# Kernel optimization log

Measured on AMD Instinct MI355X. Metric: run time of the kernel, lower is better.

The kernel has to match this reference:

```python
import jax, jax.numpy as jnp
import numpy as np

B, S, D, H, V, DFF, L, MAXLEN = 256, 64, 1024, 16, 64, 4096, 8, 64
HD = D // H
SCALE = HD ** -0.5
EPS = 1e-5


def _ln(x, g, b):
    m = jnp.mean(x, axis=-1, keepdims=True)
    v = jnp.mean((x - m) ** 2, axis=-1, keepdims=True)
    return (x - m) * jax.lax.rsqrt(v + EPS) * g + b


def setup_inputs() -> dict:
    key = jax.random.key(0)
    ks = jax.random.split(key, 12)
    n = lambda k, shape: jax.random.normal(k, shape, jnp.float32) * 0.02
    return {
        "x": jax.random.randint(ks[0], (B, S), 0, V + 1),
        "step": 0,
        "token_embed": n(ks[1], (V + 1, D)),
        "step_embed": n(ks[2], (MAXLEN, D)),
        "qkv_w": n(ks[3], (L, 3 * D, D)),
        "qkv_b": jnp.zeros((L, 3 * D), jnp.float32),
        "out_w": n(ks[4], (L, D, D)),
        "out_b": jnp.zeros((L, D), jnp.float32),
        "rel_bias": n(ks[5], (L, 2 * MAXLEN - 1)),
        "w1": n(ks[6], (L, DFF, D)),
        "b1": jnp.zeros((L, DFF), jnp.float32),
        "w2": n(ks[7], (L, D, DFF)),
        "b2": jnp.zeros((L, D), jnp.float32),
        "ln1_g": jnp.ones((L, D), jnp.float32),
        "ln1_b": jnp.zeros((L, D), jnp.float32),
        "ln2_g": jnp.ones((L, D), jnp.float32),
        "ln2_b": jnp.zeros((L, D), jnp.float32),
        "lno_g": jnp.ones((D,), jnp.float32),
        "lno_b": jnp.zeros((D,), jnp.float32),
        "pol_w": n(ks[8], (V, D)),
        "pol_b": jnp.zeros((V,), jnp.float32),
        "val_w": n(ks[9], (1, D)),
        "val_b": jnp.zeros((1,), jnp.float32),
    }


def _forward(x, step, token_embed, step_embed, qkv_w, qkv_b, out_w, out_b,
             rel_bias, w1, b1, w2, b2, ln1_g, ln1_b, ln2_g, ln2_b,
             lno_g, lno_b, pol_w, pol_b, val_w, val_b):
    h = token_embed[x]  # [B,S,D]
    step_idx = min(int(step), MAXLEN - 1)
    h = h + step_embed[step_idx][None, None, :]

    pos = jnp.arange(S)
    rel_idx = jnp.clip(pos[:, None] - pos[None, :] + (MAXLEN - 1), 0, 2 * MAXLEN - 2)  # [S,S]

    def layer(h, p):
        qw, qb, ow, ob, rb, w1_, b1_, w2_, b2_, g1, be1, g2, be2 = p
        qkv = h @ qw.T + qb  # [B,S,3D]
        qkv = qkv.reshape(B, S, 3, H, HD).transpose(2, 0, 3, 1, 4)
        q, k, v = qkv[0], qkv[1], qkv[2]  # [B,H,S,HD]
        scores = jnp.einsum('bhqd,bhkd->bhqk', q, k) * SCALE + rb[rel_idx][None, None]
        probs = jax.nn.softmax(scores, axis=-1)
        attn = jnp.einsum('bhqk,bhkd->bhqd', probs, v)  # [B,H,S,HD]
        attn = attn.transpose(0, 2, 1, 3).reshape(B, S, D) @ ow.T + ob
        h = _ln(h + attn, g1, be1)
        ffn = jax.nn.gelu(h @ w1_.T + b1_, approximate=False) @ w2_.T + b2_
        h = _ln(h + ffn, g2, be2)
        return h, None

    h, _ = jax.lax.scan(layer, h, (qkv_w, qkv_b, out_w, out_b, rel_bias,
                                   w1, b1, w2, b2, ln1_g, ln1_b, ln2_g, ln2_b))
    h = _ln(h, lno_g, lno_b)
    pooled = h.mean(axis=1)  # [B,D]
    policy = pooled @ pol_w.T + pol_b  # [B,V]
    value = pooled @ val_w.T + val_b   # [B,1]
    return policy, value, h


def reference(x, step, token_embed, step_embed, qkv_w, qkv_b, out_w, out_b,
              rel_bias, w1, b1, w2, b2, ln1_g, ln1_b, ln2_g, ln2_b,
              lno_g, lno_b, pol_w, pol_b, val_w, val_b):
    return _forward(x, step, token_embed, step_embed, qkv_w, qkv_b, out_w, out_b,
                    rel_bias, w1, b1, w2, b2, ln1_g, ln1_b, ln2_g, ln2_b,
                    lno_g, lno_b, pol_w, pol_b, val_w, val_b)
```

## Files before the change

kernel.cpp:

```cpp
#include <hip/hip_runtime.h>
#include <math.h>

typedef _Float16 f16;
typedef _Float16 f16x8 __attribute__((ext_vector_type(8)));
typedef _Float16 f16x4 __attribute__((ext_vector_type(4)));
typedef float floatx4 __attribute__((ext_vector_type(4)));

#define BATCH 256
#define SEQ 64
#define DMODEL 1024
#define NHEAD 16
#define HDIM 64
#define VOCAB 64
#define DFF 4096
#define NLAYER 8
#define MS (BATCH*SEQ)

#define GPTR(p) ((const __attribute__((address_space(1))) void*)(p))
#define LPTR(p) ((__attribute__((address_space(3))) void*)(p))

__device__ __forceinline__ floatx4 mfma16(f16x8 a, f16x8 b, floatx4 c) {
    return __builtin_amdgcn_mfma_f32_16x16x32_f16(a, b, c, 0, 0, 0);
}

__device__ __forceinline__ float gelu_f(float x) {
    return 0.5f * x * (1.f + erff(x * 0.70710678118654752f));
}

__global__ __launch_bounds__(256) void embed_k(const int* __restrict__ x, const int* __restrict__ step,
                                               const float* __restrict__ tok, const float* __restrict__ se,
                                               float* __restrict__ h, f16* __restrict__ hb) {
    int row = blockIdx.x;
    int t = threadIdx.x;
    int id = x[row];
    int si = min(max(step[0], 0), 63);
    float4 a = ((const float4*)(tok + (size_t)id * DMODEL))[t];
    float4 b = ((const float4*)(se + (size_t)si * DMODEL))[t];
    float4 o;
    o.x = a.x + b.x; o.y = a.y + b.y; o.z = a.z + b.z; o.w = a.w + b.w;
    ((float4*)(h + (size_t)row * DMODEL))[t] = o;
    f16x4 hv; hv[0] = (f16)o.x; hv[1] = (f16)o.y; hv[2] = (f16)o.z; hv[3] = (f16)o.w;
    ((f16x4*)(hb + (size_t)row * DMODEL))[t] = hv;
}

__global__ __launch_bounds__(256) void cvt_k(const float* __restrict__ src, f16* __restrict__ dst, int n4) {
    int i = blockIdx.x * 256 + threadIdx.x;
    if (i < n4) {
        float4 v = ((const float4*)src)[i];
        f16x4 o; o[0] = (f16)v.x; o[1] = (f16)v.y; o[2] = (f16)v.z; o[3] = (f16)v.w;
        ((f16x4*)dst)[i] = o;
    }
}

template<int MODE>
__global__ __launch_bounds__(256, 2) void gemm_k(const f16* __restrict__ A, const f16* __restrict__ Bw,
                                                 const float* __restrict__ bias,
                                                 f16* __restrict__ Cb, float* __restrict__ Hacc,
                                                 int M, int N, int K) {
    __shared__ f16 smem[32768];

    const int tid = threadIdx.x;
    const int lane = tid & 63;
    const int wave = tid >> 6;
    const int wm = wave >> 1, wn = wave & 1;
    const int lr = lane & 15, lg = lane >> 4;
    const int sa = lr & 7;

    const unsigned nx = gridDim.x;
    const unsigned nwg = nx * gridDim.y;
    unsigned flat = blockIdx.y * nx + blockIdx.x;
    flat = (flat & 7u) * (nwg >> 3) + (flat >> 3);
    const int m0 = (int)(flat / nx) * 128;
    const int n0 = (int)(flat % nx) * 128;

    floatx4 acc[4][4] = {};

    const int srow = tid >> 3;
    const int scbs = (tid & 7) ^ (srow & 7);
    const f16* Asrc = A + (size_t)(m0 + srow) * K + scbs * 8;
    const f16* Bsrc = Bw + (size_t)(n0 + srow) * K + scbs * 8;
    const int ldsw = wave * 512;

#define STAGE(bi, tt) do {                                                                        \
    const f16* _a = Asrc + (size_t)(tt) * 64;                                                     \
    const f16* _b = Bsrc + (size_t)(tt) * 64;                                                     \
    f16* _l = smem + ((bi) << 14) + ldsw;                                                         \
    __builtin_amdgcn_global_load_lds(GPTR(_a),                  LPTR(_l),         16, 0, 0);      \
    __builtin_amdgcn_global_load_lds(GPTR(_a + 32 * (size_t)K), LPTR(_l + 2048),  16, 0, 0);      \
    __builtin_amdgcn_global_load_lds(GPTR(_a + 64 * (size_t)K), LPTR(_l + 4096),  16, 0, 0);      \
    __builtin_amdgcn_global_load_lds(GPTR(_a + 96 * (size_t)K), LPTR(_l + 6144),  16, 0, 0);      \
    __builtin_amdgcn_global_load_lds(GPTR(_b),                  LPTR(_l + 8192),  16, 0, 0);      \
    __builtin_amdgcn_global_load_lds(GPTR(_b + 32 * (size_t)K), LPTR(_l + 10240), 16, 0, 0);      \
    __builtin_amdgcn_global_load_lds(GPTR(_b + 64 * (size_t)K), LPTR(_l + 12288), 16, 0, 0);      \
    __builtin_amdgcn_global_load_lds(GPTR(_b + 96 * (size_t)K), LPTR(_l + 14336), 16, 0, 0);      \
} while (0)

    const int NT = K >> 6;

    STAGE(0, 0);
    asm volatile("s_waitcnt vmcnt(0)" ::: "memory");
    __builtin_amdgcn_s_barrier();

    int buf = 0;
    for (int t = 0; t < NT; ++t) {
        if (t + 1 < NT) STAGE(buf ^ 1, t + 1);

        const f16* Ab = smem + (buf << 14);
        const f16* Bb = Ab + 8192;
        f16x8 af[8], bf[8];
#pragma unroll
        for (int kh = 0; kh < 2; ++kh)
#pragma unroll
            for (int mi = 0; mi < 4; ++mi)
                af[kh * 4 + mi] = *(const f16x8*)(Ab + (wm * 64 + mi * 16 + lr) * 64
                                                  + (((kh * 4 + lg) ^ sa) << 3));
#pragma unroll
        for (int kh = 0; kh < 2; ++kh)
#pragma unroll
            for (int ni = 0; ni < 4; ++ni)
                bf[kh * 4 + ni] = *(const f16x8*)(Bb + (wn * 64 + ni * 16 + lr) * 64
                                                  + (((kh * 4 + lg) ^ sa) << 3));

        __builtin_amdgcn_s_setprio(1);
#pragma unroll
        for (int kh = 0; kh < 2; ++kh)
#pragma unroll
            for (int mi = 0; mi < 4; ++mi)
#pragma unroll
                for (int ni = 0; ni < 4; ++ni)
                    acc[mi][ni] = mfma16(af[kh * 4 + mi], bf[kh * 4 + ni], acc[mi][ni]);
        __builtin_amdgcn_s_setprio(0);

        if (t + 1 < NT) { asm volatile("s_waitcnt vmcnt(0)" ::: "memory"); }
        __builtin_amdgcn_s_barrier();
        buf ^= 1;
    }
#undef STAGE

    if (MODE == 2) {
#pragma unroll
        for (int ni = 0; ni < 4; ++ni) {
            int cc = n0 + wn * 64 + ni * 16 + lr;
            float bvl = bias[cc];
#pragma unroll
            for (int mi = 0; mi < 4; ++mi)
#pragma unroll
                for (int j = 0; j < 4; ++j) {
                    int rr = m0 + wm * 64 + mi * 16 + lg * 4 + j;
                    float* p = Hacc + (size_t)rr * N + cc;
                    *p += acc[mi][ni][j] + bvl;
                }
        }
    } else {
        f16* scr = smem + wave * 4096;
        float bsv[4];
#pragma unroll
        for (int ni = 0; ni < 4; ++ni) bsv[ni] = bias[n0 + wn * 64 + ni * 16 + lr];
#pragma unroll
        for (int mi = 0; mi < 4; ++mi)
#pragma unroll
            for (int ni = 0; ni < 4; ++ni)
#pragma unroll
                for (int j = 0; j < 4; ++j) {
                    int r = mi * 16 + lg * 4 + j;
                    int c = ni * 16 + lr;
                    float v = acc[mi][ni][j] + bsv[ni];
                    if (MODE == 1) v = gelu_f(v);
                    scr[r * 64 + (((c >> 3) ^ (r & 7)) * 8) + (c & 7)] = (f16)v;
                }
        int gr = m0 + wm * 64 + lane;
        f16* dst = Cb + (size_t)gr * N + n0 + wn * 64;
#pragma unroll
        for (int i = 0; i < 8; ++i) {
            f16x8 v = *(const f16x8*)(scr + lane * 64 + ((i ^ (lane & 7)) * 8));
            *(f16x8*)(dst + i * 8) = v;
        }
    }
}

__global__ __launch_bounds__(64) void attn_k(const f16* __restrict__ qkv, const float* __restrict__ rb,
                                             f16* __restrict__ ctx) {
    const int hh = blockIdx.x;
    const int bb = blockIdx.y;
    const int lane = threadIdx.x;
    __shared__ float rbs[128];
    __shared__ f16 Vt[64][72];
    __shared__ f16 Pl[64][72];

    for (int i = lane; i < 127; i += 64) rbs[i] = rb[i];

    const f16* vrow = qkv + (size_t)(bb * 64 + lane) * 3072 + 2048 + hh * 64;
#pragma unroll
    for (int i = 0; i < 8; ++i) {
        f16x8 v = *(const f16x8*)(vrow + i * 8);
#pragma unroll
        for (int j = 0; j < 8; ++j) Vt[i * 8 + j][lane] = v[j];
    }
    __syncthreads();

    const int lr = lane & 15, lg = lane >> 4;
    floatx4 sacc[4][4] = {};
    const f16* qbase = qkv + (size_t)(bb * 64) * 3072 + hh * 64;
#pragma unroll
    for (int kk = 0; kk < 64; kk += 32) {
        f16x8 qa[4], kb[4];
#pragma unroll
        for (int mf = 0; mf < 4; ++mf)
            qa[mf] = *(const f16x8*)(qbase + (size_t)(mf * 16 + lr) * 3072 + kk + lg * 8);
#pragma unroll
        for (int nf = 0; nf < 4; ++nf)
            kb[nf] = *(const f16x8*)(qbase + 1024 + (size_t)(nf * 16 + lr) * 3072 + kk + lg * 8);
#pragma unroll
        for (int mf = 0; mf < 4; ++mf)
#pragma unroll
            for (int nf = 0; nf < 4; ++nf)
                sacc[mf][nf] = mfma16(qa[mf], kb[nf], sacc[mf][nf]);
    }

#pragma unroll
    for (int mf = 0; mf < 4; ++mf) {
#pragma unroll
        for (int j = 0; j < 4; ++j) {
            int qrow = mf * 16 + lg * 4 + j;
            float v0 = sacc[mf][0][j] * 0.125f + rbs[qrow - (0  + lr) + 63];
            float v1 = sacc[mf][1][j] * 0.125f + rbs[qrow - (16 + lr) + 63];
            float v2 = sacc[mf][2][j] * 0.125f + rbs[qrow - (32 + lr) + 63];
            float v3 = sacc[mf][3][j] * 0.125f + rbs[qrow - (48 + lr) + 63];
            float mx = fmaxf(fmaxf(v0, v1), fmaxf(v2, v3));
            for (int m = 1; m < 16; m <<= 1) mx = fmaxf(mx, __shfl_xor(mx, m));
            v0 = __expf(v0 - mx); v1 = __expf(v1 - mx); v2 = __expf(v2 - mx); v3 = __expf(v3 - mx);
            float sum = v0 + v1 + v2 + v3;
            for (int m = 1; m < 16; m <<= 1) sum += __shfl_xor(sum, m);
            float inv = 1.f / sum;
            Pl[qrow][0  + lr] = (f16)(v0 * inv);
            Pl[qrow][16 + lr] = (f16)(v1 * inv);
            Pl[qrow][32 + lr] = (f16)(v2 * inv);
            Pl[qrow][48 + lr] = (f16)(v3 * inv);
        }
    }
    __syncthreads();

    floatx4 oacc[4][4] = {};
#pragma unroll
    for (int kk = 0; kk < 64; kk += 32) {
        f16x8 pa[4], vb[4];
#pragma unroll
        for (int mf = 0; mf < 4; ++mf) pa[mf] = *(const f16x8*)&Pl[mf * 16 + lr][kk + lg * 8];
#pragma unroll
        for (int nf = 0; nf < 4; ++nf) vb[nf] = *(const f16x8*)&Vt[nf * 16 + lr][kk + lg * 8];
#pragma unroll
        for (int mf = 0; mf < 4; ++mf)
#pragma unroll
            for (int nf = 0; nf < 4; ++nf)
                oacc[mf][nf] = mfma16(pa[mf], vb[nf], oacc[mf][nf]);
    }
    __syncthreads();
#pragma unroll
    for (int mf = 0; mf < 4; ++mf)
#pragma unroll
        for (int nf = 0; nf < 4; ++nf)
#pragma unroll
            for (int j = 0; j < 4; ++j)
                Pl[mf * 16 + lg * 4 + j][nf * 16 + lr] = (f16)oacc[mf][nf][j];
    __syncthreads();
    f16* crow = ctx + (size_t)(bb * 64 + lane) * DMODEL + hh * 64;
#pragma unroll
    for (int i = 0; i < 8; ++i) {
        f16x8 v = *(const f16x8*)&Pl[lane][i * 8];
        *(f16x8*)(crow + i * 8) = v;
    }
}

__global__ __launch_bounds__(256) void ln_k(float* __restrict__ h, const float* __restrict__ g,
                                            const float* __restrict__ b, f16* __restrict__ hb, int emit) {
    int row = blockIdx.x;
    int t = threadIdx.x;
    float4 v = ((const float4*)(h + (size_t)row * DMODEL))[t];
    float s = v.x + v.y + v.z + v.w;
    float ss = v.x * v.x + v.y * v.y + v.z * v.z + v.w * v.w;
    for (int m = 1; m < 64; m <<= 1) { s += __shfl_xor(s, m); ss += __shfl_xor(ss, m); }
    __shared__ float red[8];
    if ((t & 63) == 0) { red[(t >> 6) * 2] = s; red[(t >> 6) * 2 + 1] = ss; }
    __syncthreads();
    s = red[0] + red[2] + red[4] + red[6];
    ss = red[1] + red[3] + red[5] + red[7];
    float mean = s * (1.f / 1024.f);
    float var = ss * (1.f / 1024.f) - mean * mean;
    float rstd = rsqrtf(var + 1e-5f);
    float4 gg = ((const float4*)g)[t];
    float4 bb = ((const float4*)b)[t];
    float4 o;
    o.x = (v.x - mean) * rstd * gg.x + bb.x;
    o.y = (v.y - mean) * rstd * gg.y + bb.y;
    o.z = (v.z - mean) * rstd * gg.z + bb.z;
    o.w = (v.w - mean) * rstd * gg.w + bb.w;
    ((float4*)(h + (size_t)row * DMODEL))[t] = o;
    if (emit) {
        f16x4 hv; hv[0] = (f16)o.x; hv[1] = (f16)o.y; hv[2] = (f16)o.z; hv[3] = (f16)o.w;
        ((f16x4*)(hb + (size_t)row * DMODEL))[t] = hv;
    }
}

__global__ __launch_bounds__(256) void pool_k(const float* __restrict__ h, float* __restrict__ pooled) {
    int b = blockIdx.x;
    int t = threadIdx.x;
    float sx = 0, sy = 0, sz = 0, sw = 0;
    for (int s = 0; s < SEQ; ++s) {
        float4 v = ((const float4*)(h + (size_t)(b * SEQ + s) * DMODEL))[t];
        sx += v.x; sy += v.y; sz += v.z; sw += v.w;
    }
    float4 o; o.x = sx * (1.f / 64.f); o.y = sy * (1.f / 64.f); o.z = sz * (1.f / 64.f); o.w = sw * (1.f / 64.f);
    ((float4*)(pooled + (size_t)b * DMODEL))[t] = o;
}

__global__ __launch_bounds__(64) void head_k(const float* __restrict__ pooled, const float* __restrict__ pw,
                                             const float* __restrict__ pb, const float* __restrict__ vw,
                                             const float* __restrict__ vb, float* __restrict__ out) {
    int b = blockIdx.x;
    int lane = threadIdx.x;
    const float* pr = pooled + (size_t)b * DMODEL;
    const float* wr = pw + (size_t)lane * DMODEL;
    float accp = 0.f;
    for (int d = 0; d < DMODEL; d += 4) {
        float4 x = *(const float4*)(pr + d);
        float4 w = *(const float4*)(wr + d);
        accp += x.x * w.x + x.y * w.y + x.z * w.z + x.w * w.w;
    }
    float accv = 0.f;
    for (int d = lane * 4; d < DMODEL; d += 256) {
        float4 x = *(const float4*)(pr + d);
        float4 w = *(const float4*)(vw + d);
        accv += x.x * w.x + x.y * w.y + x.z * w.z + x.w * w.w;
    }
    for (int m = 1; m < 64; m <<= 1) accv += __shfl_xor(accv, m);
    out[b * VOCAB + lane] = accp + pb[lane];
    if (lane == 0) out[BATCH * VOCAB + b] = accv + vb[0];
}

extern "C" void kernel_launch(void* const* d_in, const int* in_sizes, int n_in,
                              void* d_out, int out_size, void* d_ws, size_t ws_size,
                              hipStream_t stream) {
    const int*   x      = (const int*)d_in[0];
    const int*   step   = (const int*)d_in[1];
    const float* tok    = (const float*)d_in[2];
    const float* se     = (const float*)d_in[3];
    const float* qkv_w  = (const float*)d_in[4];
    const float* qkv_b  = (const float*)d_in[5];
    const float* out_w  = (const float*)d_in[6];
    const float* out_b  = (const float*)d_in[7];
    const float* relb   = (const float*)d_in[8];
    const float* w1     = (const float*)d_in[9];
    const float* b1     = (const float*)d_in[10];
    const float* w2     = (const float*)d_in[11];
    const float* b2     = (const float*)d_in[12];
    const float* ln1g   = (const float*)d_in[13];
    const float* ln1b   = (const float*)d_in[14];
    const float* ln2g   = (const float*)d_in[15];
    const float* ln2b   = (const float*)d_in[16];
    const float* lnog   = (const float*)d_in[17];
    const float* lnob   = (const float*)d_in[18];
    const float* pw     = (const float*)d_in[19];
    const float* pb     = (const float*)d_in[20];
    const float* vw     = (const float*)d_in[21];
    const float* vb     = (const float*)d_in[22];

    float* out = (float*)d_out;
    float* h = out + BATCH * VOCAB + BATCH;

    char* ws = (char*)d_ws;
    f16* hb     = (f16*)(ws);
    f16* uni    = (f16*)(ws + 33554432);
    f16* qkv16  = uni;
    f16* ffn16  = uni;
    f16* ctx16  = (f16*)(ws + 167772160);
    f16* wqb    = (f16*)(ws + 201326592);
    f16* wob    = (f16*)(ws + 207618048);
    f16* w1b    = (f16*)(ws + 209715200);
    f16* w2b    = (f16*)(ws + 218103808);
    float* pooled = (float*)(ws + 226492416);

    embed_k<<<MS, 256, 0, stream>>>(x, step, tok, se, h, hb);

    for (int l = 0; l < NLAYER; ++l) {
        cvt_k<<<3072, 256, 0, stream>>>(qkv_w + (size_t)l * 3145728, wqb, 786432);
        cvt_k<<<1024, 256, 0, stream>>>(out_w + (size_t)l * 1048576, wob, 262144);
        cvt_k<<<4096, 256, 0, stream>>>(w1 + (size_t)l * 4194304, w1b, 1048576);
        cvt_k<<<4096, 256, 0, stream>>>(w2 + (size_t)l * 4194304, w2b, 1048576);

        gemm_k<0><<<dim3(24, 128), 256, 0, stream>>>(hb, wqb, qkv_b + l * 3072, qkv16, nullptr, MS, 3072, 1024);
        attn_k<<<dim3(NHEAD, BATCH), 64, 0, stream>>>(qkv16, relb + l * 127, ctx16);
        gemm_k<2><<<dim3(8, 128), 256, 0, stream>>>(ctx16, wob, out_b + l * 1024, nullptr, h, MS, 1024, 1024);
        ln_k<<<MS, 256, 0, stream>>>(h, ln1g + l * 1024, ln1b + l * 1024, hb, 1);
        gemm_k<1><<<dim3(32, 128), 256, 0, stream>>>(hb, w1b, b1 + l * 4096, ffn16, nullptr, MS, 4096, 1024);
        gemm_k<2><<<dim3(8, 128), 256, 0, stream>>>(ffn16, w2b, b2 + l * 1024, nullptr, h, MS, 1024, 4096);
        ln_k<<<MS, 256, 0, stream>>>(h, ln2g + l * 1024, ln2b + l * 1024, hb, 1);
    }

    ln_k<<<MS, 256, 0, stream>>>(h, lnog, lnob, hb, 0);
    pool_k<<<BATCH, 256, 0, stream>>>(h, pooled);
    head_k<<<BATCH, 64, 0, stream>>>(pooled, pw, pb, vw, vb, out);
}
```

Baseline: 5.818 ms.

## Keep residual stream in fp16 and fuse layernorm statistics into GEMM epilogue

```diff
diff --git a/kernel.cpp b/kernel.cpp
--- a/kernel.cpp
+++ b/kernel.cpp
@@ -29,33 +29,39 @@
 
 __global__ __launch_bounds__(256) void embed_k(const int* __restrict__ x, const int* __restrict__ step,
                                                const float* __restrict__ tok, const float* __restrict__ se,
-                                               float* __restrict__ h, f16* __restrict__ hb) {
+                                               f16* __restrict__ r) {
     int row = blockIdx.x;
     int t = threadIdx.x;
     int id = x[row];
     int si = min(max(step[0], 0), 63);
     float4 a = ((const float4*)(tok + (size_t)id * DMODEL))[t];
     float4 b = ((const float4*)(se + (size_t)si * DMODEL))[t];
-    float4 o;
-    o.x = a.x + b.x; o.y = a.y + b.y; o.z = a.z + b.z; o.w = a.w + b.w;
-    ((float4*)(h + (size_t)row * DMODEL))[t] = o;
-    f16x4 hv; hv[0] = (f16)o.x; hv[1] = (f16)o.y; hv[2] = (f16)o.z; hv[3] = (f16)o.w;
-    ((f16x4*)(hb + (size_t)row * DMODEL))[t] = hv;
-}
-
-__global__ __launch_bounds__(256) void cvt_k(const float* __restrict__ src, f16* __restrict__ dst, int n4) {
-    int i = blockIdx.x * 256 + threadIdx.x;
-    if (i < n4) {
-        float4 v = ((const float4*)src)[i];
-        f16x4 o; o[0] = (f16)v.x; o[1] = (f16)v.y; o[2] = (f16)v.z; o[3] = (f16)v.w;
-        ((f16x4*)dst)[i] = o;
-    }
+    f16x4 hv; hv[0] = (f16)(a.x + b.x); hv[1] = (f16)(a.y + b.y);
+    hv[2] = (f16)(a.z + b.z); hv[3] = (f16)(a.w + b.w);
+    ((f16x4*)(r + (size_t)row * DMODEL))[t] = hv;
+}
+
+__global__ __launch_bounds__(256) void cvt4_k(const float* __restrict__ qw, const float* __restrict__ ow,
+                                              const float* __restrict__ w1, const float* __restrict__ w2,
+                                              f16* __restrict__ dq, f16* __restrict__ dO,
+                                              f16* __restrict__ d1, f16* __restrict__ d2) {
+    int gid = blockIdx.x * 256 + threadIdx.x;
+    const float4* s; f16x4* d; int off;
+    if (gid < 786432)        { s = (const float4*)qw; d = (f16x4*)dq; off = gid; }
+    else if (gid < 1048576)  { s = (const float4*)ow; d = (f16x4*)dO; off = gid - 786432; }
+    else if (gid < 2097152)  { s = (const float4*)w1; d = (f16x4*)d1; off = gid - 1048576; }
+    else                     { s = (const float4*)w2; d = (f16x4*)d2; off = gid - 2097152; }
+    float4 v = s[off];
+    f16x4 o; o[0] = (f16)v.x; o[1] = (f16)v.y; o[2] = (f16)v.z; o[3] = (f16)v.w;
+    d[off] = o;
 }
 
 template<int MODE>
 __global__ __launch_bounds__(256, 2) void gemm_k(const f16* __restrict__ A, const f16* __restrict__ Bw,
                                                  const float* __restrict__ bias,
-                                                 f16* __restrict__ Cb, float* __restrict__ Hacc,
+                                                 f16* __restrict__ Cb,
+                                                 const f16* __restrict__ Rres, f16* __restrict__ ResOut,
+                                                 float2* __restrict__ Part,
                                                  int M, int N, int K) {
     __shared__ f16 smem[32768];
 
@@ -95,61 +101,81 @@
     __builtin_amdgcn_global_load_lds(GPTR(_b + 96 * (size_t)K), LPTR(_l + 14336), 16, 0, 0);      \
 } while (0)
 
+#define TILE_BODY(t_, bi) do {                                                                    \
+    if ((t_) + 1 < NT) STAGE((bi) ^ 1, (t_) + 1);                                                 \
+    const f16* Ab = smem + ((bi) << 14);                                                          \
+    const f16* Bb = Ab + 8192;                                                                    \
+    f16x8 af[8], bf[8];                                                                           \
+    _Pragma("unroll") for (int kh = 0; kh < 2; ++kh)                                              \
+    _Pragma("unroll") for (int mi = 0; mi < 4; ++mi)                                              \
+        af[kh * 4 + mi] = *(const f16x8*)(Ab + (wm * 64 + mi * 16 + lr) * 64                      \
+                                          + (((kh * 4 + lg) ^ sa) << 3));                         \
+    _Pragma("unroll") for (int kh = 0; kh < 2; ++kh)                                              \
+    _Pragma("unroll") for (int ni = 0; ni < 4; ++ni)                                              \
+        bf[kh * 4 + ni] = *(const f16x8*)(Bb + (wn * 64 + ni * 16 + lr) * 64                      \
+                                          + (((kh * 4 + lg) ^ sa) << 3));                         \
+    __builtin_amdgcn_s_setprio(1);                                                                \
+    _Pragma("unroll") for (int kh = 0; kh < 2; ++kh)                                              \
+    _Pragma("unroll") for (int mi = 0; mi < 4; ++mi)                                              \
+    _Pragma("unroll") for (int ni = 0; ni < 4; ++ni)                                              \
+        acc[mi][ni] = mfma16(af[kh * 4 + mi], bf[kh * 4 + ni], acc[mi][ni]);                      \
+    __builtin_amdgcn_s_setprio(0);                                                                \
+    if ((t_) + 1 < NT) { asm volatile("s_waitcnt vmcnt(0)" ::: "memory"); }                       \
+    __builtin_amdgcn_s_barrier();                                                                 \
+} while (0)
+
     const int NT = K >> 6;
 
     STAGE(0, 0);
     asm volatile("s_waitcnt vmcnt(0)" ::: "memory");
     __builtin_amdgcn_s_barrier();
 
-    int buf = 0;
-    for (int t = 0; t < NT; ++t) {
-        if (t + 1 < NT) STAGE(buf ^ 1, t + 1);
-
-        const f16* Ab = smem + (buf << 14);
-        const f16* Bb = Ab + 8192;
-        f16x8 af[8], bf[8];
-#pragma unroll
-        for (int kh = 0; kh < 2; ++kh)
-#pragma unroll
-            for (int mi = 0; mi < 4; ++mi)
-                af[kh * 4 + mi] = *(const f16x8*)(Ab + (wm * 64 + mi * 16 + lr) * 64
-                                                  + (((kh * 4 + lg) ^ sa) << 3));
-#pragma unroll
-        for (int kh = 0; kh < 2; ++kh)
+    for (int t = 0; t < NT; t += 2) {
+        TILE_BODY(t, 0);
+        TILE_BODY(t + 1, 1);
+    }
+#undef STAGE
+#undef TILE_BODY
+
+    if (MODE == 2) {
+        float bsv[4];
+#pragma unroll
+        for (int ni = 0; ni < 4; ++ni) bsv[ni] = bias[n0 + wn * 64 + ni * 16 + lr];
+        f16* scr = smem + wave * 4096;
+#pragma unroll
+        for (int mi = 0; mi < 4; ++mi)
 #pragma unroll
             for (int ni = 0; ni < 4; ++ni)
-                bf[kh * 4 + ni] = *(const f16x8*)(Bb + (wn * 64 + ni * 16 + lr) * 64
-                                                  + (((kh * 4 + lg) ^ sa) << 3));
-
-        __builtin_amdgcn_s_setprio(1);
-#pragma unroll
-        for (int kh = 0; kh < 2; ++kh)
-#pragma unroll
-            for (int mi = 0; mi < 4; ++mi)
-#pragma unroll
-                for (int ni = 0; ni < 4; ++ni)
-                    acc[mi][ni] = mfma16(af[kh * 4 + mi], bf[kh * 4 + ni], acc[mi][ni]);
-        __builtin_amdgcn_s_setprio(0);
-
-        if (t + 1 < NT) { asm volatile("s_waitcnt vmcnt(0)" ::: "memory"); }
-        __builtin_amdgcn_s_barrier();
-        buf ^= 1;
-    }
-#undef STAGE
-
-    if (MODE == 2) {
-#pragma unroll
-        for (int ni = 0; ni < 4; ++ni) {
-            int cc = n0 + wn * 64 + ni * 16 + lr;
-            float bvl = bias[cc];
-#pragma unroll
-            for (int mi = 0; mi < 4; ++mi)
 #pragma unroll
                 for (int j = 0; j < 4; ++j) {
-                    int rr = m0 + wm * 64 + mi * 16 + lg * 4 + j;
-                    float* p = Hacc + (size_t)rr * N + cc;
-                    *p += acc[mi][ni][j] + bvl;
+                    int rr = mi * 16 + lg * 4 + j;
+                    int cc = ni * 16 + lr;
+                    scr[rr * 64 + (((cc >> 3) ^ (rr & 7)) * 8) + (cc & 7)]
+                        = (f16)(acc[mi][ni][j] + bsv[ni]);
                 }
+        int gr = m0 + wm * 64 + lane;
+        const f16* rrow = Rres + (size_t)gr * N + n0 + wn * 64;
+        f16* orow = ResOut + (size_t)gr * N + n0 + wn * 64;
+        float s = 0.f, ss = 0.f;
+#pragma unroll
+        for (int i = 0; i < 8; ++i) {
+            f16x8 a = *(const f16x8*)(scr + lane * 64 + ((i ^ (lane & 7)) * 8));
+            f16x8 rv = *(const f16x8*)(rrow + i * 8);
+            f16x8 o;
+#pragma unroll
+            for (int k = 0; k < 8; ++k) {
+                float v = (float)a[k] + (float)rv[k];
+                s += v; ss += v * v;
+                o[k] = (f16)v;
+            }
+            *(f16x8*)(orow + i * 8) = o;
+        }
+        float* red = (float*)(smem + 16384);
+        if (wn == 1) { red[(wm * 64 + lane) * 2] = s; red[(wm * 64 + lane) * 2 + 1] = ss; }
+        __syncthreads();
+        if (wn == 0) {
+            float s2 = red[(wm * 64 + lane) * 2], ss2 = red[(wm * 64 + lane) * 2 + 1];
+            Part[(size_t)gr * (N >> 7) + (n0 >> 7)] = float2{s + s2, ss + ss2};
         }
     } else {
         f16* scr = smem + wave * 4096;
@@ -162,11 +188,11 @@
             for (int ni = 0; ni < 4; ++ni)
 #pragma unroll
                 for (int j = 0; j < 4; ++j) {
-                    int r = mi * 16 + lg * 4 + j;
-                    int c = ni * 16 + lr;
+                    int rr = mi * 16 + lg * 4 + j;
+                    int cc = ni * 16 + lr;
                     float v = acc[mi][ni][j] + bsv[ni];
                     if (MODE == 1) v = gelu_f(v);
-                    scr[r * 64 + (((c >> 3) ^ (r & 7)) * 8) + (c & 7)] = (f16)v;
+                    scr[rr * 64 + (((cc >> 3) ^ (rr & 7)) * 8) + (cc & 7)] = (f16)v;
                 }
         int gr = m0 + wm * 64 + lane;
         f16* dst = Cb + (size_t)gr * N + n0 + wn * 64;
@@ -271,13 +297,43 @@
     }
 }
 
-__global__ __launch_bounds__(256) void ln_k(float* __restrict__ h, const float* __restrict__ g,
-                                            const float* __restrict__ b, f16* __restrict__ hb, int emit) {
+__global__ __launch_bounds__(128) void ln_k(const f16* __restrict__ res, const float2* __restrict__ part,
+                                            const float* __restrict__ g, const float* __restrict__ b,
+                                            f16* __restrict__ out) {
     int row = blockIdx.x;
     int t = threadIdx.x;
-    float4 v = ((const float4*)(h + (size_t)row * DMODEL))[t];
-    float s = v.x + v.y + v.z + v.w;
-    float ss = v.x * v.x + v.y * v.y + v.z * v.z + v.w * v.w;
+    f16x8 rv = ((const f16x8*)(res + (size_t)row * DMODEL))[t];
+    float s = 0.f, ss = 0.f;
+#pragma unroll
+    for (int c = 0; c < 8; ++c) {
+        float2 p = part[(size_t)row * 8 + c];
+        s += p.x; ss += p.y;
+    }
+    float mean = s * (1.f / 1024.f);
+    float var = ss * (1.f / 1024.f) - mean * mean;
+    float rstd = rsqrtf(var + 1e-5f);
+    float4 g0 = ((const float4*)g)[t * 2], g1 = ((const float4*)g)[t * 2 + 1];
+    float4 b0 = ((const float4*)b)[t * 2], b1 = ((const float4*)b)[t * 2 + 1];
+    f16x8 o;
+    o[0] = (f16)(((float)rv[0] - mean) * rstd * g0.x + b0.x);
+    o[1] = (f16)(((float)rv[1] - mean) * rstd * g0.y + b0.y);
+    o[2] = (f16)(((float)rv[2] - mean) * rstd * g0.z + b0.z);
+    o[3] = (f16)(((float)rv[3] - mean) * rstd * g0.w + b0.w);
+    o[4] = (f16)(((float)rv[4] - mean) * rstd * g1.x + b1.x);
+    o[5] = (f16)(((float)rv[5] - mean) * rstd * g1.y + b1.y);
+    o[6] = (f16)(((float)rv[6] - mean) * rstd * g1.z + b1.z);
+    o[7] = (f16)(((float)rv[7] - mean) * rstd * g1.w + b1.w);
+    ((f16x8*)(out + (size_t)row * DMODEL))[t] = o;
+}
+
+__global__ __launch_bounds__(256) void lnf_k(const f16* __restrict__ res, const float* __restrict__ g,
+                                             const float* __restrict__ b, float* __restrict__ h) {
+    int row = blockIdx.x;
+    int t = threadIdx.x;
+    f16x4 rv = ((const f16x4*)(res + (size_t)row * DMODEL))[t];
+    float v0 = (float)rv[0], v1 = (float)rv[1], v2 = (float)rv[2], v3 = (float)rv[3];
+    float s = v0 + v1 + v2 + v3;
+    float ss = v0 * v0 + v1 * v1 + v2 * v2 + v3 * v3;
     for (int m = 1; m < 64; m <<= 1) { s += __shfl_xor(s, m); ss += __shfl_xor(ss, m); }
     __shared__ float red[8];
     if ((t & 63) == 0) { red[(t >> 6) * 2] = s; red[(t >> 6) * 2 + 1] = ss; }
@@ -290,15 +346,11 @@
     float4 gg = ((const float4*)g)[t];
     float4 bb = ((const float4*)b)[t];
     float4 o;
-    o.x = (v.x - mean) * rstd * gg.x + bb.x;
-    o.y = (v.y - mean) * rstd * gg.y + bb.y;
-    o.z = (v.z - mean) * rstd * gg.z + bb.z;
-    o.w = (v.w - mean) * rstd * gg.w + bb.w;
+    o.x = (v0 - mean) * rstd * gg.x + bb.x;
+    o.y = (v1 - mean) * rstd * gg.y + bb.y;
+    o.z = (v2 - mean) * rstd * gg.z + bb.z;
+    o.w = (v3 - mean) * rstd * gg.w + bb.w;
     ((float4*)(h + (size_t)row * DMODEL))[t] = o;
-    if (emit) {
-        f16x4 hv; hv[0] = (f16)o.x; hv[1] = (f16)o.y; hv[2] = (f16)o.z; hv[3] = (f16)o.w;
-        ((f16x4*)(hb + (size_t)row * DMODEL))[t] = hv;
-    }
 }
 
 __global__ __launch_bounds__(256) void pool_k(const float* __restrict__ h, float* __restrict__ pooled) {
@@ -368,35 +420,39 @@
     float* h = out + BATCH * VOCAB + BATCH;
 
     char* ws = (char*)d_ws;
-    f16* hb     = (f16*)(ws);
-    f16* uni    = (f16*)(ws + 33554432);
-    f16* qkv16  = uni;
-    f16* ffn16  = uni;
+    f16* rB     = (f16*)(ws);
+    f16* resA   = (f16*)(ws + 33554432);
+    f16* qkv16  = (f16*)(ws + 67108864);
     f16* ctx16  = (f16*)(ws + 167772160);
+    f16* ffn16  = (f16*)(ws + 67108864);
     f16* wqb    = (f16*)(ws + 201326592);
     f16* wob    = (f16*)(ws + 207618048);
     f16* w1b    = (f16*)(ws + 209715200);
     f16* w2b    = (f16*)(ws + 218103808);
+    float2* part = (float2*)(ws + 226492416);
     float* pooled = (float*)(ws + 226492416);
 
-    embed_k<<<MS, 256, 0, stream>>>(x, step, tok, se, h, hb);
+    embed_k<<<MS, 256, 0, stream>>>(x, step, tok, se, rB);
 
     for (int l = 0; l < NLAYER; ++l) {
-        cvt_k<<<3072, 256, 0, stream>>>(qkv_w + (size_t)l * 3145728, wqb, 786432);
-        cvt_k<<<1024, 256, 0, stream>>>(out_w + (size_t)l * 1048576, wob, 262144);
-        cvt_k<<<4096, 256, 0, stream>>>(w1 + (size_t)l * 4194304, w1b, 1048576);
-        cvt_k<<<4096, 256, 0, stream>>>(w2 + (size_t)l * 4194304, w2b, 1048576);
-
-        gemm_k<0><<<dim3(24, 128), 256, 0, stream>>>(hb, wqb, qkv_b + l * 3072, qkv16, nullptr, MS, 3072, 1024);
+        cvt4_k<<<12288, 256, 0, stream>>>(qkv_w + (size_t)l * 3145728, out_w + (size_t)l * 1048576,
+                                          w1 + (size_t)l * 4194304, w2 + (size_t)l * 4194304,
+                                          wqb, wob, w1b, w2b);
+
+        gemm_k<0><<<dim3(24, 128), 256, 0, stream>>>(rB, wqb, qkv_b + l * 3072, qkv16,
+                                                     nullptr, nullptr, nullptr, MS, 3072, 1024);
         attn_k<<<dim3(NHEAD, BATCH), 64, 0, stream>>>(qkv16, relb + l * 127, ctx16);
-        gemm_k<2><<<dim3(8, 128), 256, 0, stream>>>(ctx16, wob, out_b + l * 1024, nullptr, h, MS, 1024, 1024);
-        ln_k<<<MS, 256, 0, stream>>>(h, ln1g + l * 1024, ln1b + l * 1024, hb, 1);
-        gemm_k<1><<<dim3(32, 128), 256, 0, stream>>>(hb, w1b, b1 + l * 4096, ffn16, nullptr, MS, 4096, 1024);
-        gemm_k<2><<<dim3(8, 128), 256, 0, stream>>>(ffn16, w2b, b2 + l * 1024, nullptr, h, MS, 1024, 4096);
-        ln_k<<<MS, 256, 0, stream>>>(h, ln2g + l * 1024, ln2b + l * 1024, hb, 1);
-    }
-
-    ln_k<<<MS, 256, 0, stream>>>(h, lnog, lnob, hb, 0);
+        gemm_k<2><<<dim3(8, 128), 256, 0, stream>>>(ctx16, wob, out_b + l * 1024, nullptr,
+                                                    rB, resA, part, MS, 1024, 1024);
+        ln_k<<<MS, 128, 0, stream>>>(resA, part, ln1g + l * 1024, ln1b + l * 1024, rB);
+        gemm_k<1><<<dim3(32, 128), 256, 0, stream>>>(rB, w1b, b1 + l * 4096, ffn16,
+                                                     nullptr, nullptr, nullptr, MS, 4096, 1024);
+        gemm_k<2><<<dim3(8, 128), 256, 0, stream>>>(ffn16, w2b, b2 + l * 1024, nullptr,
+                                                    rB, resA, part, MS, 1024, 4096);
+        ln_k<<<MS, 128, 0, stream>>>(resA, part, ln2g + l * 1024, ln2b + l * 1024, rB);
+    }
+
+    lnf_k<<<MS, 256, 0, stream>>>(rB, lnog, lnob, h);
     pool_k<<<BATCH, 256, 0, stream>>>(h, pooled);
     head_k<<<BATCH, 64, 0, stream>>>(pooled, pw, pb, vw, vb, out);
 }
```

Result: faster. 5.012 ms (-13.9%).
